# Kernel tuning notes

Hardware: AMD Instinct MI355X
Metric: run time of the kernel (lower is better)

The kernel has to match this reference:

```python
import jax, jax.numpy as jnp
import numpy as np

B, C, H, G, NCLS = 32, 256, 128, 128, 2  # graphs, nodes-per-graph==in_channels, hidden, matrix pool, classes
N = B * C                                # total nodes = 8192
E = 131072


def setup_inputs() -> dict:
    key = jax.random.key(0)
    ks = jax.random.split(key, 12)
    gain = 5.0 / 3.0
    xav = gain * np.sqrt(6.0 / (C + C))  # xavier_uniform bound for [C,C]
    return {
        "x": jax.random.normal(ks[0], (N, C), jnp.float32),
        "edge_index": jax.random.randint(ks[1], (2, E), 0, N),
        "graph_id": jax.random.randint(ks[2], (B,), 0, G),
        "batch": jnp.arange(N) // C,
        "pert_W": jax.random.uniform(ks[3], (G, C, C), jnp.float32, -xav, xav),
        "pert_b": jax.random.uniform(ks[4], (G, C, C), jnp.float32, -xav, xav),
        "mask_W": jax.random.uniform(ks[5], (G, C, C), jnp.float32, -xav, xav),
        "gcn_w0": jax.random.normal(ks[6], (C, H), jnp.float32) / np.sqrt(C),
        "gcn_w1": jax.random.normal(ks[7], (H, H), jnp.float32) / np.sqrt(H),
        "gcn_w2": jax.random.normal(ks[8], (H, H), jnp.float32) / np.sqrt(H),
        "mlp_W": jax.random.normal(ks[9], (2 * H, NCLS), jnp.float32) / np.sqrt(2 * H),
        "mlp_b": jnp.zeros((NCLS,), jnp.float32),
    }


def _hard_where(s):
    # MyWhere: 0 if s <= 0.5 else 1
    return jnp.where(s <= 0.5, 0.0, 1.0).astype(s.dtype)


def _predictor(x, adj, batch, gcn_w0, gcn_w1, gcn_w2, mlp_W, mlp_b):
    # GCN encoder: h <- relu(A @ h @ W); readout = concat(mean-pool, max-pool); MLP+sigmoid
    h = x
    for W in (gcn_w0, gcn_w1, gcn_w2):
        h = jax.nn.relu(adj @ (h @ W))
    sums = jax.ops.segment_sum(h, batch, num_segments=B)
    cnt = jax.ops.segment_sum(jnp.ones((h.shape[0], 1), h.dtype), batch, num_segments=B)
    mean = sums / jnp.maximum(cnt, 1.0)
    mx = jax.ops.segment_max(h, batch, num_segments=B)
    pooled = jnp.concatenate([mean, mx], axis=-1)  # [B, 2H]
    return jax.nn.sigmoid(pooled @ mlp_W + mlp_b)


def reference(x, edge_index, graph_id, batch, pert_W, pert_b, mask_W,
              gcn_w0, gcn_w1, gcn_w2, mlp_W, mlp_b):
    # dense adjacency (duplicate edges sum, matching sparse_coo.to_dense)
    adj = jnp.zeros((N, N), jnp.float32).at[edge_index[0], edge_index[1]].add(1.0)
    P = pert_W[graph_id]    # [B, C, C] block-diag blocks
    bias = pert_b[graph_id]  # [B, C, C] block-diag bias blocks
    # block_diag(P) @ adj == per-block GEMM over row stripes
    PA = jnp.einsum('bij,bjn->bin', P, adj.reshape(B, C, N))  # [B, C, N]
    PA = PA.reshape(B, C, B, C).at[jnp.arange(B), :, jnp.arange(B), :].add(bias)
    PA = PA.reshape(N, N)
    pert_adj = _hard_where(jax.nn.sigmoid(PA))
    M = _hard_where(jax.nn.sigmoid(mask_W[graph_id].reshape(N, C)))
    x_masked = M * x
    pred = _predictor(x, adj, batch, gcn_w0, gcn_w1, gcn_w2, mlp_W, mlp_b)
    aug_pred = _predictor(x_masked, pert_adj, batch, gcn_w0, gcn_w1, gcn_w2, mlp_W, mlp_b)
    return (adj, pert_adj, M, pred, aug_pred, x_masked)
```

## Files before the change

### kernel.cpp

```cpp
#include <hip/hip_runtime.h>
#include <hip/hip_bf16.h>

#define NN 8192
#define CC 256
#define BBg 32
#define HH 128
#define EE 131072

typedef __attribute__((ext_vector_type(8))) short short8;
typedef __attribute__((ext_vector_type(4))) float f32x4;
typedef unsigned long long ull;

__device__ __forceinline__ float hard01(float v) {
    if (v >= 1e-6f) return 1.0f;
    if (v <= 0.0f) return 0.0f;
    float ef = (float)exp(-(double)v);
    float s = 1.0f / (1.0f + ef);
    return (s > 0.5f) ? 1.0f : 0.0f;
}

__device__ __forceinline__ unsigned short f2bf(float f) {
    unsigned u = __float_as_uint(f);
    u += 0x7FFFu + ((u >> 16) & 1u);
    return (unsigned short)(u >> 16);
}
__device__ __forceinline__ float bf2f(unsigned short b) {
    return __uint_as_float(((unsigned)b) << 16);
}

__global__ void k_hist(const int* __restrict__ ei, int* __restrict__ rowcnt,
                       int* __restrict__ colcnt, unsigned char* __restrict__ coljs) {
    int e = blockIdx.x * 256 + threadIdx.x;
    if (e >= EE) return;
    int r = ei[e], c = ei[EE + e];
    atomicAdd(&rowcnt[r], 1);
    int idx = (r >> 8) * NN + c;
    int slot = atomicAdd(&colcnt[idx], 1);
    if (slot < 16) coljs[(size_t)idx * 16 + slot] = (unsigned char)(r & 255);
}

__global__ void k_scan(const int* __restrict__ rowcnt, int* __restrict__ rowptr,
                       int* __restrict__ rowfill) {
    __shared__ int sums[256];
    int t = threadIdx.x;
    int base = t * 32;
    int loc[32];
    int s = 0;
    #pragma unroll
    for (int i = 0; i < 32; ++i) { loc[i] = s; s += rowcnt[base + i]; }
    sums[t] = s;
    __syncthreads();
    if (t == 0) {
        int a = 0;
        for (int i = 0; i < 256; ++i) { int v = sums[i]; sums[i] = a; a += v; }
        rowptr[NN] = a;
    }
    __syncthreads();
    int off = sums[t];
    #pragma unroll
    for (int i = 0; i < 32; ++i) {
        rowptr[base + i] = off + loc[i];
        rowfill[base + i] = off + loc[i];
    }
}

__global__ void k_fill(const int* __restrict__ ei, int* __restrict__ rowfill,
                       int* __restrict__ csrcol) {
    int e = blockIdx.x * 256 + threadIdx.x;
    if (e >= EE) return;
    int r = ei[e], c = ei[EE + e];
    int pos = atomicAdd(&rowfill[r], 1);
    csrcol[pos] = c;
}

__global__ void __launch_bounds__(256) k_adj_write(const int* __restrict__ rowptr,
                                                   const int* __restrict__ csrcol,
                                                   float* __restrict__ adj) {
    __shared__ int cnt[NN];
    int row = blockIdx.x, t = threadIdx.x;
    int4 z = make_int4(0, 0, 0, 0);
    #pragma unroll
    for (int i = 0; i < 8; ++i) *(int4*)&cnt[(i * 256 + t) * 4] = z;
    __syncthreads();
    int start = rowptr[row], end = rowptr[row + 1];
    for (int e = start + t; e < end; e += 256) atomicAdd(&cnt[csrcol[e]], 1);
    __syncthreads();
    float* dst = adj + (size_t)row * NN;
    #pragma unroll
    for (int i = 0; i < 8; ++i) {
        int p = i * 1024 + t * 4;
        float4 f;
        f.x = (float)cnt[p + 0]; f.y = (float)cnt[p + 1];
        f.z = (float)cnt[p + 2]; f.w = (float)cnt[p + 3];
        *(float4*)(dst + p) = f;
    }
}

__global__ void k_mask(const float* __restrict__ maskW, const int* __restrict__ gid,
                       const float* __restrict__ x, float* __restrict__ Mo,
                       float* __restrict__ xm) {
    int i = blockIdx.x * 256 + threadIdx.x;
    int base = i * 4;
    int r = base >> 8;
    int c = base & 255;
    int g = gid[r >> 8];
    float4 mv = *(const float4*)(maskW + ((size_t)g << 16) + ((size_t)(r & 255) << 8) + c);
    float4 xv = *(const float4*)(x + ((size_t)r << 8) + c);
    float4 m, o;
    m.x = hard01(mv.x); m.y = hard01(mv.y); m.z = hard01(mv.z); m.w = hard01(mv.w);
    o.x = m.x * xv.x; o.y = m.y * xv.y; o.z = m.z * xv.z; o.w = m.w * xv.w;
    *(float4*)(Mo + ((size_t)r << 8) + c) = m;
    *(float4*)(xm + ((size_t)r << 8) + c) = o;
}

__global__ void __launch_bounds__(256) k_pertadj(const float* __restrict__ pertW,
                                                 const float* __restrict__ pertB,
                                                 const int* __restrict__ gid,
                                                 const int* __restrict__ colcnt,
                                                 const unsigned char* __restrict__ coljs,
                                                 float* __restrict__ padj,
                                                 unsigned char* __restrict__ padjbits) {
    __shared__ float Pl[32][257];
    int nc = blockIdx.x & 3, rt = (blockIdx.x >> 2) & 7, b = blockIdx.x >> 5;
    int t = threadIdx.x;
    int g = gid[b];
    const float* src = pertW + ((size_t)g << 16) + (size_t)rt * 32 * CC;
    #pragma unroll 4
    for (int i = 0; i < 32; ++i) Pl[i][t] = src[i * CC + t];
    __syncthreads();
    int ty = t >> 6, tx = t & 63;
    int ro = ty * 8;
    const float* bsrc = pertB + ((size_t)g << 16) + (size_t)(rt * 32 + ro) * CC;
    for (int it = 0; it < 4; ++it) {
        unsigned bits[8];
        #pragma unroll
        for (int ii = 0; ii < 8; ++ii) bits[ii] = 0;
        #pragma unroll
        for (int half = 0; half < 2; ++half) {
            int n = nc * 2048 + it * 512 + tx * 8 + half * 4;
            int cidx = b * NN + n;
            int4 cnt4 = *(const int4*)(colcnt + cidx);
            const uint4* jp = (const uint4*)(coljs + (size_t)cidx * 16);
            float s[8][4];
            #pragma unroll
            for (int ii = 0; ii < 8; ++ii)
                #pragma unroll
                for (int cc = 0; cc < 4; ++cc) s[ii][cc] = 0.0f;
            #pragma unroll
            for (int cc = 0; cc < 4; ++cc) {
                int cnt = (&cnt4.x)[cc];
                cnt = cnt > 16 ? 16 : cnt;
                if (cnt == 0) continue;
                uint4 jv = jp[cc];
                for (int q = 0; q < cnt; ++q) {
                    unsigned word = (q < 8) ? ((q < 4) ? jv.x : jv.y)
                                            : ((q < 12) ? jv.z : jv.w);
                    int j = (word >> ((q & 3) * 8)) & 255;
                    #pragma unroll
                    for (int ii = 0; ii < 8; ++ii) s[ii][cc] += Pl[ro + ii][j];
                }
            }
            bool diag = ((n >> 8) == b);
            #pragma unroll
            for (int ii = 0; ii < 8; ++ii) {
                float4 v = make_float4(s[ii][0], s[ii][1], s[ii][2], s[ii][3]);
                if (diag) {
                    float4 bv = *(const float4*)(bsrc + (size_t)ii * CC + (n & 255));
                    v.x += bv.x; v.y += bv.y; v.z += bv.z; v.w += bv.w;
                }
                float4 f;
                f.x = hard01(v.x); f.y = hard01(v.y); f.z = hard01(v.z); f.w = hard01(v.w);
                size_t ob = (size_t)(b * CC + rt * 32 + ro + ii) * NN + n;
                *(float4*)(padj + ob) = f;
                unsigned nib = (f.x != 0.f ? 1u : 0u) | (f.y != 0.f ? 2u : 0u) |
                               (f.z != 0.f ? 4u : 0u) | (f.w != 0.f ? 8u : 0u);
                bits[ii] |= nib << (half * 4);
            }
        }
        #pragma unroll
        for (int ii = 0; ii < 8; ++ii) {
            size_t bb = (size_t)(b * CC + rt * 32 + ro + ii) * (NN / 8)
                        + nc * 256 + it * 64 + tx;
            padjbits[bb] = (unsigned char)bits[ii];
        }
    }
}

__global__ void __launch_bounds__(256) k_gemm_dual(const float* __restrict__ Ap,
                                                   const float* __restrict__ Aa,
                                                   const float* __restrict__ W,
                                                   float* __restrict__ Zp,
                                                   unsigned short* __restrict__ Zthi,
                                                   unsigned short* __restrict__ Ztlo,
                                                   int K, int relu, int aparts, int apstride) {
    __shared__ float Alp[32][68];
    __shared__ float Ala[32][68];
    __shared__ float Wl[64][132];
    int mt = blockIdx.x;
    int t = threadIdx.x;
    int ty = t >> 3, tx = t & 7;
    float accp[16], acca[16];
    #pragma unroll
    for (int u = 0; u < 16; ++u) { accp[u] = 0.0f; acca[u] = 0.0f; }
    for (int kc = 0; kc < K; kc += 64) {
        int row = t >> 3, q = t & 7;
        {
            const float* ap = Ap + (size_t)(mt * 32 + row) * K + kc + q * 8;
            float4 f0 = *(const float4*)ap;
            float4 f1 = *(const float4*)(ap + 4);
            if (relu) {
                f0.x = fmaxf(f0.x, 0.f); f0.y = fmaxf(f0.y, 0.f);
                f0.z = fmaxf(f0.z, 0.f); f0.w = fmaxf(f0.w, 0.f);
                f1.x = fmaxf(f1.x, 0.f); f1.y = fmaxf(f1.y, 0.f);
                f1.z = fmaxf(f1.z, 0.f); f1.w = fmaxf(f1.w, 0.f);
            }
            *(float4*)&Alp[row][q * 8] = f0;
            *(float4*)&Alp[row][q * 8 + 4] = f1;
        }
        {
            const float* ap = Aa + (size_t)(mt * 32 + row) * K + kc + q * 8;
            float4 f0 = *(const float4*)ap;
            float4 f1 = *(const float4*)(ap + 4);
            for (int p = 1; p < aparts; ++p) {
                float4 g0 = *(const float4*)(ap + (size_t)p * apstride);
                float4 g1 = *(const float4*)(ap + (size_t)p * apstride + 4);
                f0.x += g0.x; f0.y += g0.y; f0.z += g0.z; f0.w += g0.w;
                f1.x += g1.x; f1.y += g1.y; f1.z += g1.z; f1.w += g1.w;
            }
            if (relu) {
                f0.x = fmaxf(f0.x, 0.f); f0.y = fmaxf(f0.y, 0.f);
                f0.z = fmaxf(f0.z, 0.f); f0.w = fmaxf(f0.w, 0.f);
                f1.x = fmaxf(f1.x, 0.f); f1.y = fmaxf(f1.y, 0.f);
                f1.z = fmaxf(f1.z, 0.f); f1.w = fmaxf(f1.w, 0.f);
            }
            *(float4*)&Ala[row][q * 8] = f0;
            *(float4*)&Ala[row][q * 8 + 4] = f1;
        }
        {
            int wrow = t >> 2, wq = t & 3;
            const float* wp = W + (size_t)(kc + wrow) * HH + wq * 32;
            #pragma unroll
            for (int u = 0; u < 32; u += 4)
                *(float4*)&Wl[wrow][wq * 32 + u] = *(const float4*)(wp + u);
        }
        __syncthreads();
        #pragma unroll 2
        for (int kk = 0; kk < 64; ++kk) {
            float a = Alp[ty][kk];
            float b2 = Ala[ty][kk];
            #pragma unroll
            for (int u = 0; u < 16; u += 4) {
                float4 wv = *(const float4*)(&Wl[kk][tx * 16 + u]);
                accp[u + 0] += a * wv.x; accp[u + 1] += a * wv.y;
                accp[u + 2] += a * wv.z; accp[u + 3] += a * wv.w;
                acca[u + 0] += b2 * wv.x; acca[u + 1] += b2 * wv.y;
                acca[u + 2] += b2 * wv.z; acca[u + 3] += b2 * wv.w;
            }
        }
        __syncthreads();
    }
    {
        float* cp = Zp + (size_t)(mt * 32 + ty) * HH + tx * 16;
        #pragma unroll
        for (int u = 0; u < 16; u += 4) {
            float4 f;
            f.x = accp[u]; f.y = accp[u + 1]; f.z = accp[u + 2]; f.w = accp[u + 3];
            *(float4*)(cp + u) = f;
        }
    }
    {
        __syncthreads();
        float* Tl = &Wl[0][0];
        #pragma unroll
        for (int u = 0; u < 16; ++u) Tl[ty * 132 + tx * 16 + u] = acca[u];
        __syncthreads();
        int col = t >> 1, half = t & 1;
        unsigned short hu[16] __attribute__((aligned(16)));
        unsigned short lu[16] __attribute__((aligned(16)));
        #pragma unroll
        for (int rr = 0; rr < 16; ++rr) {
            float v = Tl[(half * 16 + rr) * 132 + col];
            unsigned short hb = f2bf(v);
            hu[rr] = hb;
            lu[rr] = f2bf(v - bf2f(hb));
        }
        size_t ob = (size_t)col * NN + mt * 32 + half * 16;
        *(uint4*)(Zthi + ob)     = *(const uint4*)&hu[0];
        *(uint4*)(Zthi + ob + 8) = *(const uint4*)&hu[8];
        *(uint4*)(Ztlo + ob)     = *(const uint4*)&lu[0];
        *(uint4*)(Ztlo + ob + 8) = *(const uint4*)&lu[8];
    }
}

__global__ void k_spmm_gather(const int* __restrict__ rowptr,
                              const int* __restrict__ csrcol,
                              const float* __restrict__ Z,
                              float* __restrict__ S) {
    int t = threadIdx.x;
    int row = blockIdx.x * 2 + (t >> 7);
    int col = t & 127;
    int start = rowptr[row], end = rowptr[row + 1];
    float s = 0.f;
    if (start < end) {
        int c = csrcol[start];
        for (int e = start; e < end; ++e) {
            int cn = (e + 1 < end) ? csrcol[e + 1] : 0;
            s += Z[(size_t)c * HH + col];
            c = cn;
        }
    }
    S[(size_t)row * HH + col] = s;
}

__global__ void __launch_bounds__(256) k_mfma_spmm(const unsigned char* __restrict__ padjbits,
                                                   const unsigned short* __restrict__ Zthi,
                                                   const unsigned short* __restrict__ Ztlo,
                                                   float* __restrict__ Sp) {
    __shared__ unsigned short Bh[128 * 72];
    __shared__ unsigned short Bl[128 * 72];
    int mt = blockIdx.x >> 3, sk = blockIdx.x & 7;
    int t = threadIdx.x, w = t >> 6, lane = t & 63;
    int quad = lane >> 4, l15 = lane & 15;
    f32x4 acc[2][8];
    #pragma unroll
    for (int m = 0; m < 2; ++m)
        #pragma unroll
        for (int i = 0; i < 8; ++i) acc[m][i] = (f32x4){0.f, 0.f, 0.f, 0.f};
    int bn = t >> 1, bq = t & 1;
    const unsigned short* zh = Zthi + (size_t)bn * NN + bq * 32;
    const unsigned short* zl = Ztlo + (size_t)bn * NN + bq * 32;
    int row0 = mt * 128 + w * 32 + l15;
    const ull* ab0 = (const ull*)(padjbits + (size_t)row0 * (NN / 8) + sk * 128);
    const ull* ab1 = (const ull*)(padjbits + (size_t)(row0 + 16) * (NN / 8) + sk * 128);
    int ldsw = bn * 72 + bq * 32;
    int bmb = l15 * 72 + quad * 8;
    for (int st = 0; st < 16; ++st) {
        int k = sk * 1024 + st * 64;
        ull bits0 = ab0[st];
        ull bits1 = ab1[st];
        *(uint4*)(Bh + ldsw + 0)  = *(const uint4*)(zh + k);
        *(uint4*)(Bh + ldsw + 8)  = *(const uint4*)(zh + k + 8);
        *(uint4*)(Bh + ldsw + 16) = *(const uint4*)(zh + k + 16);
        *(uint4*)(Bh + ldsw + 24) = *(const uint4*)(zh + k + 24);
        *(uint4*)(Bl + ldsw + 0)  = *(const uint4*)(zl + k);
        *(uint4*)(Bl + ldsw + 8)  = *(const uint4*)(zl + k + 8);
        *(uint4*)(Bl + ldsw + 16) = *(const uint4*)(zl + k + 16);
        *(uint4*)(Bl + ldsw + 24) = *(const uint4*)(zl + k + 24);
        __syncthreads();
        #pragma unroll
        for (int ksub = 0; ksub < 2; ++ksub) {
            unsigned b0 = ((unsigned)(bits0 >> (ksub * 32)) >> (quad * 8)) & 0xFFu;
            unsigned b1 = ((unsigned)(bits1 >> (ksub * 32)) >> (quad * 8)) & 0xFFu;
            short8 a0, a1;
            #pragma unroll
            for (int j = 0; j < 8; ++j) {
                a0[j] = (b0 & (1u << j)) ? (short)0x3F80 : (short)0;
                a1[j] = (b1 & (1u << j)) ? (short)0x3F80 : (short)0;
            }
            #pragma unroll
            for (int nt = 0; nt < 8; ++nt) {
                short8 fh = *(const short8*)(Bh + nt * 16 * 72 + bmb + ksub * 32);
                short8 fl = *(const short8*)(Bl + nt * 16 * 72 + bmb + ksub * 32);
                acc[0][nt] = __builtin_amdgcn_mfma_f32_16x16x32_bf16(a0, fh, acc[0][nt], 0, 0, 0);
                acc[0][nt] = __builtin_amdgcn_mfma_f32_16x16x32_bf16(a0, fl, acc[0][nt], 0, 0, 0);
                acc[1][nt] = __builtin_amdgcn_mfma_f32_16x16x32_bf16(a1, fh, acc[1][nt], 0, 0, 0);
                acc[1][nt] = __builtin_amdgcn_mfma_f32_16x16x32_bf16(a1, fl, acc[1][nt], 0, 0, 0);
            }
        }
        __syncthreads();
    }
    int dc = l15, dr = quad * 4;
    float* base = Sp + (size_t)sk * NN * HH + (size_t)(mt * 128 + w * 32 + dr) * HH;
    #pragma unroll
    for (int m = 0; m < 2; ++m)
        #pragma unroll
        for (int nt = 0; nt < 8; ++nt)
            #pragma unroll
            for (int r = 0; r < 4; ++r)
                base[(size_t)(m * 16 + r) * HH + nt * 16 + dc] = acc[m][nt][r];
}

__global__ void __launch_bounds__(256) k_pool2(const float* __restrict__ S,
                                               const float* __restrict__ Sp,
                                               const float* __restrict__ mlpW,
                                               const float* __restrict__ mlpb,
                                               float* __restrict__ pred,
                                               float* __restrict__ augp,
                                               int apstride) {
    __shared__ float ps[256], pm[256], pl[256], r0[256], r1[256];
    int aug = blockIdx.x >> 5, g = blockIdx.x & 31, t = threadIdx.x;
    const float* Sb = aug ? Sp : S;
    int parts = aug ? 8 : 1;
    float* outp = aug ? augp : pred;
    int col = t & 127, half = t >> 7;
    const float* base = Sb + (size_t)(g * CC + half * 128) * HH + col;
    float sum = 0.f, mx = -3.0e38f;
    for (int rr = 0; rr < 128; ++rr) {
        float v = base[(size_t)rr * HH];
        for (int p = 1; p < parts; ++p) v += base[(size_t)p * apstride + (size_t)rr * HH];
        v = fmaxf(v, 0.f);
        sum += v;
        mx = fmaxf(mx, v);
    }
    ps[t] = sum; pm[t] = mx;
    __syncthreads();
    if (half == 0) {
        pl[col] = (ps[col] + ps[col + 128]) * (1.0f / 256.0f);
        pl[col + 128] = fmaxf(pm[col], pm[col + 128]);
    }
    __syncthreads();
    r0[t] = pl[t] * mlpW[t * 2 + 0];
    r1[t] = pl[t] * mlpW[t * 2 + 1];
    __syncthreads();
    for (int sft = 128; sft > 0; sft >>= 1) {
        if (t < sft) { r0[t] += r0[t + sft]; r1[t] += r1[t + sft]; }
        __syncthreads();
    }
    if (t == 0) {
        float l0 = r0[0] + mlpb[0];
        float l1 = r1[0] + mlpb[1];
        outp[g * 2 + 0] = 1.0f / (1.0f + expf(-l0));
        outp[g * 2 + 1] = 1.0f / (1.0f + expf(-l1));
    }
}

extern "C" void kernel_launch(void* const* d_in, const int* in_sizes, int n_in,
                              void* d_out, int out_size, void* d_ws, size_t ws_size,
                              hipStream_t stream) {
    (void)in_sizes; (void)n_in; (void)out_size; (void)ws_size;
    const float* x     = (const float*)d_in[0];
    const int*   ei    = (const int*)d_in[1];
    const int*   gid   = (const int*)d_in[2];
    const float* pertW = (const float*)d_in[4];
    const float* pertB = (const float*)d_in[5];
    const float* maskW = (const float*)d_in[6];
    const float* w0    = (const float*)d_in[7];
    const float* w1    = (const float*)d_in[8];
    const float* w2    = (const float*)d_in[9];
    const float* mlpW  = (const float*)d_in[10];
    const float* mlpb  = (const float*)d_in[11];

    float* out  = (float*)d_out;
    float* adj  = out;
    float* padj = out + (size_t)NN * NN;
    float* Mo   = out + 2 * (size_t)NN * NN;
    float* pred = Mo + (size_t)NN * CC;
    float* augp = pred + (size_t)BBg * 2;
    float* xm   = augp + (size_t)BBg * 2;

    char* ws = (char*)d_ws;
    int*            colcnt   = (int*)ws;
    int*            rowcnt   = (int*)(ws + (1 << 20));
    int*            rowptr   = (int*)(ws + (1 << 20) + (64 << 10));
    int*            rowfill  = (int*)(ws + (1 << 20) + (128 << 10));
    unsigned char*  coljs    = (unsigned char*)(ws + (2 << 20));
    int*            csrcol   = (int*)(ws + (6 << 20));
    float*          Z        = (float*)(ws + (7 << 20));
    float*          S        = (float*)(ws + (11 << 20));
    unsigned short* Zthi     = (unsigned short*)(ws + (15 << 20));
    unsigned short* Ztlo     = (unsigned short*)(ws + (17 << 20));
    float*          Sp       = (float*)(ws + (19 << 20));
    unsigned char*  padjbits = (unsigned char*)(ws + (51 << 20));
    const int PS = NN * HH;

    hipMemsetAsync(colcnt, 0, (1 << 20) + (32 << 10), stream);
    k_hist<<<EE / 256, 256, 0, stream>>>(ei, rowcnt, colcnt, coljs);
    k_scan<<<1, 256, 0, stream>>>(rowcnt, rowptr, rowfill);
    k_fill<<<EE / 256, 256, 0, stream>>>(ei, rowfill, csrcol);
    k_adj_write<<<NN, 256, 0, stream>>>(rowptr, csrcol, adj);
    k_mask<<<(NN * CC / 4) / 256, 256, 0, stream>>>(maskW, gid, x, Mo, xm);
    k_pertadj<<<1024, 256, 0, stream>>>(pertW, pertB, gid, colcnt, coljs, padj, padjbits);

    k_gemm_dual<<<256, 256, 0, stream>>>(x, xm, w0, Z, Zthi, Ztlo, 256, 0, 1, 0);
    k_spmm_gather<<<NN / 2, 256, 0, stream>>>(rowptr, csrcol, Z, S);
    k_mfma_spmm<<<512, 256, 0, stream>>>(padjbits, Zthi, Ztlo, Sp);
    k_gemm_dual<<<256, 256, 0, stream>>>(S, Sp, w1, Z, Zthi, Ztlo, 128, 1, 8, PS);
    k_spmm_gather<<<NN / 2, 256, 0, stream>>>(rowptr, csrcol, Z, S);
    k_mfma_spmm<<<512, 256, 0, stream>>>(padjbits, Zthi, Ztlo, Sp);
    k_gemm_dual<<<256, 256, 0, stream>>>(S, Sp, w2, Z, Zthi, Ztlo, 128, 1, 8, PS);
    k_spmm_gather<<<NN / 2, 256, 0, stream>>>(rowptr, csrcol, Z, S);
    k_mfma_spmm<<<512, 256, 0, stream>>>(padjbits, Zthi, Ztlo, Sp);
    k_pool2<<<64, 256, 0, stream>>>(S, Sp, mlpW, mlpb, pred, augp, PS);
}
```

Measured before the change: 1.104 ms.

## Merge independent kernels into combined launches via block-index dispatch

Independent stages are merged into shared launches that branch on block index: histogram with mask, scan with perturbed-adjacency build, first GEMM with CSR fill, and MFMA SpMM with gather SpMM and the dense adjacency write. This cuts the launch count from 16 to 9 and lets work that does not depend on each other run concurrently, filling the GPU better during the small serial stages. In exchange, heterogeneous blocks share one kernel's register and LDS allocation. The adjacency write also moves later in the schedule, and the one-block scan now runs alongside a thousand pertadj blocks.

```diff
diff --git a/kernel.cpp b/kernel.cpp
--- a/kernel.cpp
+++ b/kernel.cpp
@@ -28,101 +28,69 @@
     return __uint_as_float(((unsigned)b) << 16);
 }
 
-__global__ void k_hist(const int* __restrict__ ei, int* __restrict__ rowcnt,
-                       int* __restrict__ colcnt, unsigned char* __restrict__ coljs) {
-    int e = blockIdx.x * 256 + threadIdx.x;
-    if (e >= EE) return;
-    int r = ei[e], c = ei[EE + e];
-    atomicAdd(&rowcnt[r], 1);
-    int idx = (r >> 8) * NN + c;
-    int slot = atomicAdd(&colcnt[idx], 1);
-    if (slot < 16) coljs[(size_t)idx * 16 + slot] = (unsigned char)(r & 255);
-}
-
-__global__ void k_scan(const int* __restrict__ rowcnt, int* __restrict__ rowptr,
-                       int* __restrict__ rowfill) {
+__global__ void k_hist_mask(const int* __restrict__ ei, int* __restrict__ rowcnt,
+                            int* __restrict__ colcnt, unsigned char* __restrict__ coljs,
+                            const float* __restrict__ maskW, const int* __restrict__ gid,
+                            const float* __restrict__ x, float* __restrict__ Mo,
+                            float* __restrict__ xm) {
+    int blk = blockIdx.x, t = threadIdx.x;
+    if (blk < 512) {
+        int e = blk * 256 + t;
+        int r = ei[e], c = ei[EE + e];
+        atomicAdd(&rowcnt[r], 1);
+        int idx = (r >> 8) * NN + c;
+        int slot = atomicAdd(&colcnt[idx], 1);
+        if (slot < 16) coljs[(size_t)idx * 16 + slot] = (unsigned char)(r & 255);
+    } else {
+        int i = (blk - 512) * 256 + t;
+        int base = i * 4;
+        int r = base >> 8;
+        int c = base & 255;
+        int g = gid[r >> 8];
+        float4 mv = *(const float4*)(maskW + ((size_t)g << 16) + ((size_t)(r & 255) << 8) + c);
+        float4 xv = *(const float4*)(x + ((size_t)r << 8) + c);
+        float4 m, o;
+        m.x = hard01(mv.x); m.y = hard01(mv.y); m.z = hard01(mv.z); m.w = hard01(mv.w);
+        o.x = m.x * xv.x; o.y = m.y * xv.y; o.z = m.z * xv.z; o.w = m.w * xv.w;
+        *(float4*)(Mo + ((size_t)r << 8) + c) = m;
+        *(float4*)(xm + ((size_t)r << 8) + c) = o;
+    }
+}
+
+__global__ void __launch_bounds__(256) k_scan_pertadj(
+        const int* __restrict__ rowcnt, int* __restrict__ rowptr,
+        int* __restrict__ rowfill,
+        const float* __restrict__ pertW, const float* __restrict__ pertB,
+        const int* __restrict__ gid, const int* __restrict__ colcnt,
+        const unsigned char* __restrict__ coljs,
+        float* __restrict__ padj, unsigned char* __restrict__ padjbits) {
+    __shared__ float Pl[32][257];
     __shared__ int sums[256];
     int t = threadIdx.x;
-    int base = t * 32;
-    int loc[32];
-    int s = 0;
-    #pragma unroll
-    for (int i = 0; i < 32; ++i) { loc[i] = s; s += rowcnt[base + i]; }
-    sums[t] = s;
-    __syncthreads();
-    if (t == 0) {
-        int a = 0;
-        for (int i = 0; i < 256; ++i) { int v = sums[i]; sums[i] = a; a += v; }
-        rowptr[NN] = a;
-    }
-    __syncthreads();
-    int off = sums[t];
-    #pragma unroll
-    for (int i = 0; i < 32; ++i) {
-        rowptr[base + i] = off + loc[i];
-        rowfill[base + i] = off + loc[i];
-    }
-}
-
-__global__ void k_fill(const int* __restrict__ ei, int* __restrict__ rowfill,
-                       int* __restrict__ csrcol) {
-    int e = blockIdx.x * 256 + threadIdx.x;
-    if (e >= EE) return;
-    int r = ei[e], c = ei[EE + e];
-    int pos = atomicAdd(&rowfill[r], 1);
-    csrcol[pos] = c;
-}
-
-__global__ void __launch_bounds__(256) k_adj_write(const int* __restrict__ rowptr,
-                                                   const int* __restrict__ csrcol,
-                                                   float* __restrict__ adj) {
-    __shared__ int cnt[NN];
-    int row = blockIdx.x, t = threadIdx.x;
-    int4 z = make_int4(0, 0, 0, 0);
-    #pragma unroll
-    for (int i = 0; i < 8; ++i) *(int4*)&cnt[(i * 256 + t) * 4] = z;
-    __syncthreads();
-    int start = rowptr[row], end = rowptr[row + 1];
-    for (int e = start + t; e < end; e += 256) atomicAdd(&cnt[csrcol[e]], 1);
-    __syncthreads();
-    float* dst = adj + (size_t)row * NN;
-    #pragma unroll
-    for (int i = 0; i < 8; ++i) {
-        int p = i * 1024 + t * 4;
-        float4 f;
-        f.x = (float)cnt[p + 0]; f.y = (float)cnt[p + 1];
-        f.z = (float)cnt[p + 2]; f.w = (float)cnt[p + 3];
-        *(float4*)(dst + p) = f;
-    }
-}
-
-__global__ void k_mask(const float* __restrict__ maskW, const int* __restrict__ gid,
-                       const float* __restrict__ x, float* __restrict__ Mo,
-                       float* __restrict__ xm) {
-    int i = blockIdx.x * 256 + threadIdx.x;
-    int base = i * 4;
-    int r = base >> 8;
-    int c = base & 255;
-    int g = gid[r >> 8];
-    float4 mv = *(const float4*)(maskW + ((size_t)g << 16) + ((size_t)(r & 255) << 8) + c);
-    float4 xv = *(const float4*)(x + ((size_t)r << 8) + c);
-    float4 m, o;
-    m.x = hard01(mv.x); m.y = hard01(mv.y); m.z = hard01(mv.z); m.w = hard01(mv.w);
-    o.x = m.x * xv.x; o.y = m.y * xv.y; o.z = m.z * xv.z; o.w = m.w * xv.w;
-    *(float4*)(Mo + ((size_t)r << 8) + c) = m;
-    *(float4*)(xm + ((size_t)r << 8) + c) = o;
-}
-
-__global__ void __launch_bounds__(256) k_pertadj(const float* __restrict__ pertW,
-                                                 const float* __restrict__ pertB,
-                                                 const int* __restrict__ gid,
-                                                 const int* __restrict__ colcnt,
-                                                 const unsigned char* __restrict__ coljs,
-                                                 float* __restrict__ padj,
-                                                 unsigned char* __restrict__ padjbits) {
-    __shared__ float Pl[32][257];
-    int nc = blockIdx.x & 3, rt = (blockIdx.x >> 2) & 7, b = blockIdx.x >> 5;
-    int t = threadIdx.x;
+    if (blockIdx.x == 0) {
+        int base = t * 32;
+        int loc[32];
+        int s = 0;
+        #pragma unroll
+        for (int i = 0; i < 32; ++i) { loc[i] = s; s += rowcnt[base + i]; }
+        sums[t] = s;
+        __syncthreads();
+        if (t == 0) {
+            int a = 0;
+            for (int i = 0; i < 256; ++i) { int v = sums[i]; sums[i] = a; a += v; }
+            rowptr[NN] = a;
+        }
+        __syncthreads();
+        int off = sums[t];
+        #pragma unroll
+        for (int i = 0; i < 32; ++i) {
+            rowptr[base + i] = off + loc[i];
+            rowfill[base + i] = off + loc[i];
+        }
+        return;
+    }
+    int bid = blockIdx.x - 1;
+    int nc = bid & 3, rt = (bid >> 2) & 7, b = bid >> 5;
     int g = gid[b];
     const float* src = pertW + ((size_t)g << 16) + (size_t)rt * 32 * CC;
     #pragma unroll 4
@@ -186,18 +154,13 @@
     }
 }
 
-__global__ void __launch_bounds__(256) k_gemm_dual(const float* __restrict__ Ap,
-                                                   const float* __restrict__ Aa,
-                                                   const float* __restrict__ W,
-                                                   float* __restrict__ Zp,
-                                                   unsigned short* __restrict__ Zthi,
-                                                   unsigned short* __restrict__ Ztlo,
-                                                   int K, int relu, int aparts, int apstride) {
-    __shared__ float Alp[32][68];
-    __shared__ float Ala[32][68];
-    __shared__ float Wl[64][132];
-    int mt = blockIdx.x;
-    int t = threadIdx.x;
+__device__ __forceinline__ void gemm_dual_body(
+        int mt, int t,
+        const float* __restrict__ Ap, const float* __restrict__ Aa,
+        const float* __restrict__ W, float* __restrict__ Zp,
+        unsigned short* __restrict__ Zthi, unsigned short* __restrict__ Ztlo,
+        int K, int relu, int aparts, int apstride,
+        float (*Alp)[68], float (*Ala)[68], float (*Wl)[132]) {
     int ty = t >> 3, tx = t & 7;
     float accp[16], acca[16];
     #pragma unroll
@@ -292,92 +255,148 @@
     }
 }
 
-__global__ void k_spmm_gather(const int* __restrict__ rowptr,
-                              const int* __restrict__ csrcol,
-                              const float* __restrict__ Z,
-                              float* __restrict__ S) {
-    int t = threadIdx.x;
-    int row = blockIdx.x * 2 + (t >> 7);
-    int col = t & 127;
-    int start = rowptr[row], end = rowptr[row + 1];
-    float s = 0.f;
-    if (start < end) {
-        int c = csrcol[start];
-        for (int e = start; e < end; ++e) {
-            int cn = (e + 1 < end) ? csrcol[e + 1] : 0;
-            s += Z[(size_t)c * HH + col];
-            c = cn;
-        }
-    }
-    S[(size_t)row * HH + col] = s;
-}
-
-__global__ void __launch_bounds__(256) k_mfma_spmm(const unsigned char* __restrict__ padjbits,
-                                                   const unsigned short* __restrict__ Zthi,
-                                                   const unsigned short* __restrict__ Ztlo,
-                                                   float* __restrict__ Sp) {
-    __shared__ unsigned short Bh[128 * 72];
-    __shared__ unsigned short Bl[128 * 72];
-    int mt = blockIdx.x >> 3, sk = blockIdx.x & 7;
-    int t = threadIdx.x, w = t >> 6, lane = t & 63;
-    int quad = lane >> 4, l15 = lane & 15;
-    f32x4 acc[2][8];
-    #pragma unroll
-    for (int m = 0; m < 2; ++m)
-        #pragma unroll
-        for (int i = 0; i < 8; ++i) acc[m][i] = (f32x4){0.f, 0.f, 0.f, 0.f};
-    int bn = t >> 1, bq = t & 1;
-    const unsigned short* zh = Zthi + (size_t)bn * NN + bq * 32;
-    const unsigned short* zl = Ztlo + (size_t)bn * NN + bq * 32;
-    int row0 = mt * 128 + w * 32 + l15;
-    const ull* ab0 = (const ull*)(padjbits + (size_t)row0 * (NN / 8) + sk * 128);
-    const ull* ab1 = (const ull*)(padjbits + (size_t)(row0 + 16) * (NN / 8) + sk * 128);
-    int ldsw = bn * 72 + bq * 32;
-    int bmb = l15 * 72 + quad * 8;
-    for (int st = 0; st < 16; ++st) {
-        int k = sk * 1024 + st * 64;
-        ull bits0 = ab0[st];
-        ull bits1 = ab1[st];
-        *(uint4*)(Bh + ldsw + 0)  = *(const uint4*)(zh + k);
-        *(uint4*)(Bh + ldsw + 8)  = *(const uint4*)(zh + k + 8);
-        *(uint4*)(Bh + ldsw + 16) = *(const uint4*)(zh + k + 16);
-        *(uint4*)(Bh + ldsw + 24) = *(const uint4*)(zh + k + 24);
-        *(uint4*)(Bl + ldsw + 0)  = *(const uint4*)(zl + k);
-        *(uint4*)(Bl + ldsw + 8)  = *(const uint4*)(zl + k + 8);
-        *(uint4*)(Bl + ldsw + 16) = *(const uint4*)(zl + k + 16);
-        *(uint4*)(Bl + ldsw + 24) = *(const uint4*)(zl + k + 24);
-        __syncthreads();
-        #pragma unroll
-        for (int ksub = 0; ksub < 2; ++ksub) {
-            unsigned b0 = ((unsigned)(bits0 >> (ksub * 32)) >> (quad * 8)) & 0xFFu;
-            unsigned b1 = ((unsigned)(bits1 >> (ksub * 32)) >> (quad * 8)) & 0xFFu;
-            short8 a0, a1;
-            #pragma unroll
-            for (int j = 0; j < 8; ++j) {
-                a0[j] = (b0 & (1u << j)) ? (short)0x3F80 : (short)0;
-                a1[j] = (b1 & (1u << j)) ? (short)0x3F80 : (short)0;
-            }
-            #pragma unroll
-            for (int nt = 0; nt < 8; ++nt) {
-                short8 fh = *(const short8*)(Bh + nt * 16 * 72 + bmb + ksub * 32);
-                short8 fl = *(const short8*)(Bl + nt * 16 * 72 + bmb + ksub * 32);
-                acc[0][nt] = __builtin_amdgcn_mfma_f32_16x16x32_bf16(a0, fh, acc[0][nt], 0, 0, 0);
-                acc[0][nt] = __builtin_amdgcn_mfma_f32_16x16x32_bf16(a0, fl, acc[0][nt], 0, 0, 0);
-                acc[1][nt] = __builtin_amdgcn_mfma_f32_16x16x32_bf16(a1, fh, acc[1][nt], 0, 0, 0);
-                acc[1][nt] = __builtin_amdgcn_mfma_f32_16x16x32_bf16(a1, fl, acc[1][nt], 0, 0, 0);
-            }
-        }
-        __syncthreads();
-    }
-    int dc = l15, dr = quad * 4;
-    float* base = Sp + (size_t)sk * NN * HH + (size_t)(mt * 128 + w * 32 + dr) * HH;
-    #pragma unroll
-    for (int m = 0; m < 2; ++m)
-        #pragma unroll
-        for (int nt = 0; nt < 8; ++nt)
-            #pragma unroll
-            for (int r = 0; r < 4; ++r)
-                base[(size_t)(m * 16 + r) * HH + nt * 16 + dc] = acc[m][nt][r];
+__global__ void __launch_bounds__(256) k_gemm_fill(
+        const float* __restrict__ Ap, const float* __restrict__ Aa,
+        const float* __restrict__ W, float* __restrict__ Zp,
+        unsigned short* __restrict__ Zthi, unsigned short* __restrict__ Ztlo,
+        int K, int relu, int aparts, int apstride,
+        const int* __restrict__ ei, int* __restrict__ rowfill,
+        int* __restrict__ csrcol) {
+    __shared__ float Alp[32][68];
+    __shared__ float Ala[32][68];
+    __shared__ float Wl[64][132];
+    int blk = blockIdx.x, t = threadIdx.x;
+    if (blk < 256) {
+        gemm_dual_body(blk, t, Ap, Aa, W, Zp, Zthi, Ztlo, K, relu, aparts, apstride,
+                       Alp, Ala, Wl);
+    } else {
+        int e = (blk - 256) * 256 + t;
+        int r = ei[e], c = ei[EE + e];
+        int pos = atomicAdd(&rowfill[r], 1);
+        csrcol[pos] = c;
+    }
+}
+
+__global__ void __launch_bounds__(256) k_gemm_dual(
+        const float* __restrict__ Ap, const float* __restrict__ Aa,
+        const float* __restrict__ W, float* __restrict__ Zp,
+        unsigned short* __restrict__ Zthi, unsigned short* __restrict__ Ztlo,
+        int K, int relu, int aparts, int apstride) {
+    __shared__ float Alp[32][68];
+    __shared__ float Ala[32][68];
+    __shared__ float Wl[64][132];
+    gemm_dual_body(blockIdx.x, threadIdx.x, Ap, Aa, W, Zp, Zthi, Ztlo,
+                   K, relu, aparts, apstride, Alp, Ala, Wl);
+}
+
+__global__ void __launch_bounds__(256) k_layer(
+        const unsigned char* __restrict__ padjbits,
+        const unsigned short* __restrict__ Zthi,
+        const unsigned short* __restrict__ Ztlo,
+        float* __restrict__ Sp,
+        const int* __restrict__ rowptr, const int* __restrict__ csrcol,
+        const float* __restrict__ Z, float* __restrict__ S,
+        float* __restrict__ adj, int adjrows) {
+    __shared__ __align__(16) char sm[128 * 72 * 2 * 2];
+    int blk = blockIdx.x, t = threadIdx.x;
+    if (blk < 512) {
+        unsigned short* Bh = (unsigned short*)sm;
+        unsigned short* Bl = (unsigned short*)(sm + 128 * 72 * 2);
+        int mt = blk >> 3, sk = blk & 7;
+        int w = t >> 6, lane = t & 63;
+        int quad = lane >> 4, l15 = lane & 15;
+        f32x4 acc[2][8];
+        #pragma unroll
+        for (int m = 0; m < 2; ++m)
+            #pragma unroll
+            for (int i = 0; i < 8; ++i) acc[m][i] = (f32x4){0.f, 0.f, 0.f, 0.f};
+        int bn = t >> 1, bq = t & 1;
+        const unsigned short* zh = Zthi + (size_t)bn * NN + bq * 32;
+        const unsigned short* zl = Ztlo + (size_t)bn * NN + bq * 32;
+        int row0 = mt * 128 + w * 32 + l15;
+        const ull* ab0 = (const ull*)(padjbits + (size_t)row0 * (NN / 8) + sk * 128);
+        const ull* ab1 = (const ull*)(padjbits + (size_t)(row0 + 16) * (NN / 8) + sk * 128);
+        int ldsw = bn * 72 + bq * 32;
+        int bmb = l15 * 72 + quad * 8;
+        for (int st = 0; st < 16; ++st) {
+            int k = sk * 1024 + st * 64;
+            ull bits0 = ab0[st];
+            ull bits1 = ab1[st];
+            *(uint4*)(Bh + ldsw + 0)  = *(const uint4*)(zh + k);
+            *(uint4*)(Bh + ldsw + 8)  = *(const uint4*)(zh + k + 8);
+            *(uint4*)(Bh + ldsw + 16) = *(const uint4*)(zh + k + 16);
+            *(uint4*)(Bh + ldsw + 24) = *(const uint4*)(zh + k + 24);
+            *(uint4*)(Bl + ldsw + 0)  = *(const uint4*)(zl + k);
+            *(uint4*)(Bl + ldsw + 8)  = *(const uint4*)(zl + k + 8);
+            *(uint4*)(Bl + ldsw + 16) = *(const uint4*)(zl + k + 16);
+            *(uint4*)(Bl + ldsw + 24) = *(const uint4*)(zl + k + 24);
+            __syncthreads();
+            #pragma unroll
+            for (int ksub = 0; ksub < 2; ++ksub) {
+                unsigned b0 = ((unsigned)(bits0 >> (ksub * 32)) >> (quad * 8)) & 0xFFu;
+                unsigned b1 = ((unsigned)(bits1 >> (ksub * 32)) >> (quad * 8)) & 0xFFu;
+                short8 a0, a1;
+                #pragma unroll
+                for (int j = 0; j < 8; ++j) {
+                    a0[j] = (b0 & (1u << j)) ? (short)0x3F80 : (short)0;
+                    a1[j] = (b1 & (1u << j)) ? (short)0x3F80 : (short)0;
+                }
+                #pragma unroll
+                for (int nt = 0; nt < 8; ++nt) {
+                    short8 fh = *(const short8*)(Bh + nt * 16 * 72 + bmb + ksub * 32);
+                    short8 fl = *(const short8*)(Bl + nt * 16 * 72 + bmb + ksub * 32);
+                    acc[0][nt] = __builtin_amdgcn_mfma_f32_16x16x32_bf16(a0, fh, acc[0][nt], 0, 0, 0);
+                    acc[0][nt] = __builtin_amdgcn_mfma_f32_16x16x32_bf16(a0, fl, acc[0][nt], 0, 0, 0);
+                    acc[1][nt] = __builtin_amdgcn_mfma_f32_16x16x32_bf16(a1, fh, acc[1][nt], 0, 0, 0);
+                    acc[1][nt] = __builtin_amdgcn_mfma_f32_16x16x32_bf16(a1, fl, acc[1][nt], 0, 0, 0);
+                }
+            }
+            __syncthreads();
+        }
+        int dc = l15, dr = quad * 4;
+        float* base = Sp + (size_t)sk * NN * HH + (size_t)(mt * 128 + w * 32 + dr) * HH;
+        #pragma unroll
+        for (int m = 0; m < 2; ++m)
+            #pragma unroll
+            for (int nt = 0; nt < 8; ++nt)
+                #pragma unroll
+                for (int r = 0; r < 4; ++r)
+                    base[(size_t)(m * 16 + r) * HH + nt * 16 + dc] = acc[m][nt][r];
+    } else if (blk < 4608) {
+        int bid = blk - 512;
+        int row = bid * 2 + (t >> 7);
+        int col = t & 127;
+        int start = rowptr[row], end = rowptr[row + 1];
+        float s = 0.f;
+        if (start < end) {
+            int c = csrcol[start];
+            for (int e = start; e < end; ++e) {
+                int cn = (e + 1 < end) ? csrcol[e + 1] : 0;
+                s += Z[(size_t)c * HH + col];
+                c = cn;
+            }
+        }
+        S[(size_t)row * HH + col] = s;
+    } else {
+        int* cnt = (int*)sm;
+        int row = blk - 4608;
+        int4 z = make_int4(0, 0, 0, 0);
+        #pragma unroll
+        for (int i = 0; i < 8; ++i) *(int4*)&cnt[(i * 256 + t) * 4] = z;
+        __syncthreads();
+        int start = rowptr[row], end = rowptr[row + 1];
+        for (int e = start + t; e < end; e += 256) atomicAdd(&cnt[csrcol[e]], 1);
+        __syncthreads();
+        float* dst = adj + (size_t)row * NN;
+        #pragma unroll
+        for (int i = 0; i < 8; ++i) {
+            int p = i * 1024 + t * 4;
+            float4 f;
+            f.x = (float)cnt[p + 0]; f.y = (float)cnt[p + 1];
+            f.z = (float)cnt[p + 2]; f.w = (float)cnt[p + 3];
+            *(float4*)(dst + p) = f;
+        }
+    }
 }
 
 __global__ void __launch_bounds__(256) k_pool2(const float* __restrict__ S,
@@ -464,21 +483,20 @@
     const int PS = NN * HH;
 
     hipMemsetAsync(colcnt, 0, (1 << 20) + (32 << 10), stream);
-    k_hist<<<EE / 256, 256, 0, stream>>>(ei, rowcnt, colcnt, coljs);
-    k_scan<<<1, 256, 0, stream>>>(rowcnt, rowptr, rowfill);
-    k_fill<<<EE / 256, 256, 0, stream>>>(ei, rowfill, csrcol);
-    k_adj_write<<<NN, 256, 0, stream>>>(rowptr, csrcol, adj);
-    k_mask<<<(NN * CC / 4) / 256, 256, 0, stream>>>(maskW, gid, x, Mo, xm);
-    k_pertadj<<<1024, 256, 0, stream>>>(pertW, pertB, gid, colcnt, coljs, padj, padjbits);
-
-    k_gemm_dual<<<256, 256, 0, stream>>>(x, xm, w0, Z, Zthi, Ztlo, 256, 0, 1, 0);
-    k_spmm_gather<<<NN / 2, 256, 0, stream>>>(rowptr, csrcol, Z, S);
-    k_mfma_spmm<<<512, 256, 0, stream>>>(padjbits, Zthi, Ztlo, Sp);
+    k_hist_mask<<<512 + 2048, 256, 0, stream>>>(ei, rowcnt, colcnt, coljs,
+                                                maskW, gid, x, Mo, xm);
+    k_scan_pertadj<<<1025, 256, 0, stream>>>(rowcnt, rowptr, rowfill,
+                                             pertW, pertB, gid, colcnt, coljs,
+                                             padj, padjbits);
+    k_gemm_fill<<<768, 256, 0, stream>>>(x, xm, w0, Z, Zthi, Ztlo, 256, 0, 1, 0,
+                                         ei, rowfill, csrcol);
+    k_layer<<<512 + 4096 + 8192, 256, 0, stream>>>(padjbits, Zthi, Ztlo, Sp,
+                                                   rowptr, csrcol, Z, S, adj, NN);
     k_gemm_dual<<<256, 256, 0, stream>>>(S, Sp, w1, Z, Zthi, Ztlo, 128, 1, 8, PS);
-    k_spmm_gather<<<NN / 2, 256, 0, stream>>>(rowptr, csrcol, Z, S);
-    k_mfma_spmm<<<512, 256, 0, stream>>>(padjbits, Zthi, Ztlo, Sp);
+    k_layer<<<512 + 4096, 256, 0, stream>>>(padjbits, Zthi, Ztlo, Sp,
+                                            rowptr, csrcol, Z, S, adj, 0);
     k_gemm_dual<<<256, 256, 0, stream>>>(S, Sp, w2, Z, Zthi, Ztlo, 128, 1, 8, PS);
-    k_spmm_gather<<<NN / 2, 256, 0, stream>>>(rowptr, csrcol, Z, S);
-    k_mfma_spmm<<<512, 256, 0, stream>>>(padjbits, Zthi, Ztlo, Sp);
+    k_layer<<<512 + 4096, 256, 0, stream>>>(padjbits, Zthi, Ztlo, Sp,
+                                            rowptr, csrcol, Z, S, adj, 0);
     k_pool2<<<64, 256, 0, stream>>>(S, Sp, mlpW, mlpb, pred, augp, PS);
 }
```

Result: slower. 1.179 ms (+6.7%).
